# Kernel tuning notes

Measured on AMD Instinct MI355X. Metric: run time of the kernel, lower is better.

Reference implementation:

```python
import jax, jax.numpy as jnp
import numpy as np

D_MODEL = 1024
N_HEAD = 16
HEAD_DIM = D_MODEL // N_HEAD
BS, SEQ = 4, 2048
NEG_INF = -1e9


def setup_inputs() -> dict:
    key = jax.random.key(0)
    ks = jax.random.split(key, 10)
    X = jax.random.normal(ks[0], (BS, SEQ, D_MODEL), dtype=jnp.float32)
    kpm = jax.random.randint(ks[1], (BS, SEQ), 0, 2, dtype=jnp.int32)
    kpm = kpm.at[:, 0].set(0)  # guarantee at least one attendable key per batch
    scale = 1.0 / np.sqrt(D_MODEL)
    WQ = jax.random.normal(ks[2], (D_MODEL, D_MODEL), dtype=jnp.float32) * scale
    bQ = jnp.zeros((D_MODEL,), dtype=jnp.float32)
    WK = jax.random.normal(ks[3], (D_MODEL, D_MODEL), dtype=jnp.float32) * scale
    bK = jnp.zeros((D_MODEL,), dtype=jnp.float32)
    WV = jax.random.normal(ks[4], (D_MODEL, D_MODEL), dtype=jnp.float32) * scale
    bV = jnp.zeros((D_MODEL,), dtype=jnp.float32)
    WO = jax.random.normal(ks[5], (D_MODEL, D_MODEL), dtype=jnp.float32) * scale
    bO = jnp.zeros((D_MODEL,), dtype=jnp.float32)
    return {"X": X, "key_padding_mask": kpm, "WQ": WQ, "bQ": bQ,
            "WK": WK, "bK": bK, "WV": WV, "bV": bV, "WO": WO, "bO": bO}


def reference(X, key_padding_mask, WQ, bQ, WK, bK, WV, bV, WO, bO):
    bs, L, _ = X.shape
    # separate Q/K/V linear projections (torch Linear: x @ W.T + b)
    Q = X @ WQ.T + bQ
    K = X @ WK.T + bK
    V = X @ WV.T + bV
    # split heads: (bs, L, H, Dh) -> (bs, H, L, Dh)
    Q = Q.reshape(bs, L, N_HEAD, HEAD_DIM).transpose(0, 2, 1, 3)
    K = K.reshape(bs, L, N_HEAD, HEAD_DIM).transpose(0, 2, 1, 3)
    V = V.reshape(bs, L, N_HEAD, HEAD_DIM).transpose(0, 2, 1, 3)
    # scaled dot-product attention
    scores = jnp.einsum('bhqd,bhkd->bhqk', Q, K) / jnp.sqrt(
        jnp.asarray(HEAD_DIM, dtype=Q.dtype))
    # key padding mask: non-zero => ignore that key
    mask = (key_padding_mask != 0)[:, None, None, :]  # (bs,1,1,L)
    scores = jnp.where(mask, NEG_INF, scores)
    attn = jax.nn.softmax(scores, axis=-1)
    out = jnp.einsum('bhqk,bhkd->bhqd', attn, V)
    # merge heads
    out = out.transpose(0, 2, 1, 3).reshape(bs, L, D_MODEL)
    return out @ WO.T + bO
```

## Files before the change

### kernel.cpp

```cpp
#include <hip/hip_runtime.h>
#include <stdint.h>

#define BS_   4
#define SEQ_  2048
#define DM_   1024
#define NH_   16
#define DH_   64
#define MTOK_ (BS_*SEQ_)

typedef __attribute__((ext_vector_type(8))) short bf16x8;
typedef __attribute__((ext_vector_type(4))) float f32x4;

#define SA_ 0.18033688011112042f
#define SHIFT_ 16.0f

__device__ __forceinline__ unsigned short f2bf(float f) {
    union { float f; uint32_t u; } v; v.f = f;
    uint32_t r = v.u + 0x7fffu + ((v.u >> 16) & 1u);
    return (unsigned short)(r >> 16);
}

__device__ __forceinline__ float fexp2(float x) {
#if __has_builtin(__builtin_amdgcn_exp2f)
    return __builtin_amdgcn_exp2f(x);
#else
    return __expf(x * 0.69314718055994531f);
#endif
}

__device__ __forceinline__ uint32_t cvt_pk_bf16(float lo, float hi) {
    uint32_t r;
    asm("v_cvt_pk_bf16_f32 %0, %1, %2" : "=v"(r) : "v"(lo), "v"(hi));
    return r;
}

__device__ __forceinline__ void gload_lds16(const void* g, void* l) {
    __builtin_amdgcn_global_load_lds(
        (const __attribute__((address_space(1))) void*)g,
        (__attribute__((address_space(3))) void*)l, 16, 0, 0);
}

__global__ void cvt_kernel(const float* __restrict__ src,
                           unsigned short* __restrict__ dst, int n) {
    int i = (blockIdx.x * blockDim.x + threadIdx.x) * 4;
    const int stride = gridDim.x * blockDim.x * 4;
    for (; i < n; i += stride) {
        float4 v = *(const float4*)(src + i);
        ushort4 o;
        o.x = f2bf(v.x); o.y = f2bf(v.y); o.z = f2bf(v.z); o.w = f2bf(v.w);
        *(ushort4*)(dst + i) = o;
    }
}

__global__ void cvt4_kernel(const float* __restrict__ s0, const float* __restrict__ s1,
                            const float* __restrict__ s2, const float* __restrict__ s3,
                            unsigned short* __restrict__ dst) {
    const int i = (blockIdx.x * blockDim.x + threadIdx.x) * 4;
    const int mat = i >> 20;
    const int off = i & ((1 << 20) - 1);
    const float* s = (mat == 0) ? s0 : (mat == 1) ? s1 : (mat == 2) ? s2 : s3;
    float4 v = *(const float4*)(s + off);
    ushort4 o;
    o.x = f2bf(v.x); o.y = f2bf(v.y); o.z = f2bf(v.z); o.w = f2bf(v.w);
    *(ushort4*)(dst + i) = o;
}

template<int MODE>
__global__ __launch_bounds__(256) void gemm_bt(
    const unsigned short* __restrict__ A,
    const unsigned short* __restrict__ B,
    int Ndim, int Kdim,
    const float* __restrict__ bias0,
    const float* __restrict__ bias1,
    const float* __restrict__ bias2,
    unsigned short* __restrict__ Qo,
    unsigned short* __restrict__ Ko,
    unsigned short* __restrict__ Vt,
    float* __restrict__ Co)
{
    __shared__ unsigned short As[128 * 32];
    __shared__ unsigned short Bs[128 * 32];

    const int t    = threadIdx.x;
    const int lane = t & 63;
    const int w    = t >> 6;
    const int wr   = w >> 1, wc = w & 1;
    const int g    = lane >> 4, li = lane & 15;

    const int ntile = Ndim >> 7;
    const int per   = gridDim.x >> 3;
    const int sw    = (blockIdx.x & 7) * per + (blockIdx.x >> 3);
    const int tm = sw / ntile;
    const int tn = sw % ntile;

    const unsigned short* Ab = A + (size_t)tm * 128 * Kdim;
    const unsigned short* Bb = B + (size_t)tn * 128 * Kdim;

    f32x4 acc[4][4];
    const f32x4 zero = {0.f, 0.f, 0.f, 0.f};
    #pragma unroll
    for (int i = 0; i < 4; ++i)
        #pragma unroll
        for (int j = 0; j < 4; ++j)
            acc[i][j] = zero;

    const int s0 = t, s1 = t + 256;
    const int r0 = s0 >> 2, c0 = (s0 & 3) << 3;
    const int r1 = s1 >> 2, c1 = (s1 & 3) << 3;

    for (int k0 = 0; k0 < Kdim; k0 += 32) {
        gload_lds16(Ab + (size_t)r0 * Kdim + k0 + c0, (char*)As + s0 * 16);
        gload_lds16(Ab + (size_t)r1 * Kdim + k0 + c1, (char*)As + s1 * 16);
        gload_lds16(Bb + (size_t)r0 * Kdim + k0 + c0, (char*)Bs + s0 * 16);
        gload_lds16(Bb + (size_t)r1 * Kdim + k0 + c1, (char*)Bs + s1 * 16);
        __syncthreads();

        bf16x8 a[4], b[4];
        #pragma unroll
        for (int mi = 0; mi < 4; ++mi)
            a[mi] = *(const bf16x8*)&As[(wr * 64 + mi * 16 + li) * 32 + g * 8];
        #pragma unroll
        for (int ni = 0; ni < 4; ++ni)
            b[ni] = *(const bf16x8*)&Bs[(wc * 64 + ni * 16 + li) * 32 + g * 8];

        #pragma unroll
        for (int mi = 0; mi < 4; ++mi)
            #pragma unroll
            for (int ni = 0; ni < 4; ++ni)
                acc[mi][ni] = __builtin_amdgcn_mfma_f32_16x16x32_bf16(
                    a[mi], b[ni], acc[mi][ni], 0, 0, 0);
        __syncthreads();
    }

    if constexpr (MODE == 0) {
        #pragma unroll
        for (int mi = 0; mi < 4; ++mi) {
            const int gm0 = tm * 128 + wr * 64 + mi * 16 + g * 4;
            const int bb  = gm0 >> 11;
            const int l0  = gm0 & (SEQ_ - 1);
            #pragma unroll
            for (int ni = 0; ni < 4; ++ni) {
                const int gn  = tn * 128 + wc * 64 + ni * 16 + li;
                const int mat = gn >> 10;
                const int c   = gn & (DM_ - 1);
                const int hh  = c >> 6;
                const int dd  = c & (DH_ - 1);
                const float bias = (mat == 0 ? bias0 : (mat == 1 ? bias1 : bias2))[c];
                const f32x4 v = acc[mi][ni];
                if (mat == 2) {
                    const int lp = (l0 & ~31) | ((l0 & 12) << 1) | ((l0 & 16) >> 2);
                    ushort4 o;
                    o.x = f2bf(v[0] + bias);
                    o.y = f2bf(v[1] + bias);
                    o.z = f2bf(v[2] + bias);
                    o.w = f2bf(v[3] + bias);
                    *(ushort4*)&Vt[((size_t)(bb * NH_ + hh) * DH_ + dd) * SEQ_ + lp] = o;
                } else {
                    unsigned short* dst = (mat == 0) ? Qo : Ko;
                    #pragma unroll
                    for (int r = 0; r < 4; ++r)
                        dst[((size_t)(bb * NH_ + hh) * SEQ_ + l0 + r) * DH_ + dd] =
                            f2bf(v[r] + bias);
                }
            }
        }
    } else {
        #pragma unroll
        for (int mi = 0; mi < 4; ++mi) {
            const int gm0 = tm * 128 + wr * 64 + mi * 16 + g * 4;
            #pragma unroll
            for (int ni = 0; ni < 4; ++ni) {
                const int gn = tn * 128 + wc * 64 + ni * 16 + li;
                const float bias = bias0[gn];
                #pragma unroll
                for (int r = 0; r < 4; ++r)
                    Co[(size_t)(gm0 + r) * Ndim + gn] = acc[mi][ni][r] + bias;
            }
        }
    }
}

#define KPAD 72

__global__ __launch_bounds__(256) void attn_kernel(
    const unsigned short* __restrict__ Q,
    const unsigned short* __restrict__ K,
    const unsigned short* __restrict__ Vt,
    const int* __restrict__ kpm,
    unsigned short* __restrict__ Oo)
{
    __shared__ unsigned short Ks[64 * KPAD];
    __shared__ unsigned short Vs[64 * KPAD];
    __shared__ float maskLds[64];

    const int t    = threadIdx.x;
    const int lane = t & 63;
    const int w    = t >> 6;
    const int g    = lane >> 4, li = lane & 15;

    const int bh = ((blockIdx.x >> 7) << 3) + (blockIdx.x & 7);
    const int qt = (blockIdx.x >> 3) & 15;
    const int b  = bh >> 4;
    const int h  = bh & 15;
    const int q0 = qt * 128 + w * 32;

    bf16x8 qf[2][2];
    #pragma unroll
    for (int qi = 0; qi < 2; ++qi)
        #pragma unroll
        for (int kk = 0; kk < 2; ++kk)
            qf[qi][kk] = *(const bf16x8*)&Q[((size_t)bh * SEQ_ + q0 + qi * 16 + li) * DH_
                                            + kk * 32 + g * 8];

    f32x4 Oacc[2][4];
    const f32x4 zero = {0.f, 0.f, 0.f, 0.f};
    #pragma unroll
    for (int qi = 0; qi < 2; ++qi)
        #pragma unroll
        for (int di = 0; di < 4; ++di)
            Oacc[qi][di] = zero;

    float lrun[2] = {0.f, 0.f};

    const int sr = t >> 3;
    const int sc = (t & 7) * 8;

    bf16x8 kreg0, kreg1, vreg0, vreg1;
    float mreg = 0.f;

    auto load_tile = [&](int kv) {
        kreg0 = *(const bf16x8*)&K[((size_t)bh * SEQ_ + kv + sr) * DH_ + sc];
        kreg1 = *(const bf16x8*)&K[((size_t)bh * SEQ_ + kv + sr + 32) * DH_ + sc];
        vreg0 = *(const bf16x8*)&Vt[((size_t)bh * DH_ + sr) * SEQ_ + kv + sc];
        vreg1 = *(const bf16x8*)&Vt[((size_t)bh * DH_ + sr + 32) * SEQ_ + kv + sc];
        if (t < 64) mreg = (kpm[b * SEQ_ + kv + t] ? -1e9f : 0.0f) - SHIFT_;
    };
    auto store_tile = [&]() {
        *(bf16x8*)&Ks[sr * KPAD + sc] = kreg0;
        *(bf16x8*)&Ks[(sr + 32) * KPAD + sc] = kreg1;
        *(bf16x8*)&Vs[sr * KPAD + sc] = vreg0;
        *(bf16x8*)&Vs[(sr + 32) * KPAD + sc] = vreg1;
        if (t < 64) maskLds[t] = mreg;
    };

    load_tile(0);
    store_tile();

    for (int kv = 0; kv < SEQ_; kv += 64) {
        __syncthreads();
        const bool more = (kv + 64) < SEQ_;
        if (more) load_tile(kv + 64);

        float4 mk[4];
        #pragma unroll
        for (int ni = 0; ni < 4; ++ni)
            mk[ni] = *(const float4*)&maskLds[ni * 16 + g * 4];

        f32x4 sacc[2][4];
        #pragma unroll
        for (int qi = 0; qi < 2; ++qi)
            #pragma unroll
            for (int ni = 0; ni < 4; ++ni)
                sacc[qi][ni] = zero;
        __builtin_amdgcn_s_setprio(1);
        #pragma unroll
        for (int ni = 0; ni < 4; ++ni) {
            #pragma unroll
            for (int kk = 0; kk < 2; ++kk) {
                bf16x8 kb = *(const bf16x8*)&Ks[(ni * 16 + li) * KPAD + kk * 32 + g * 8];
                sacc[0][ni] = __builtin_amdgcn_mfma_f32_16x16x32_bf16(
                    kb, qf[0][kk], sacc[0][ni], 0, 0, 0);
                sacc[1][ni] = __builtin_amdgcn_mfma_f32_16x16x32_bf16(
                    kb, qf[1][kk], sacc[1][ni], 0, 0, 0);
            }
        }
        __builtin_amdgcn_s_setprio(0);

        #pragma unroll
        for (int qi = 0; qi < 2; ++qi) {
            float rs = 0.f;
            #pragma unroll
            for (int ni = 0; ni < 4; ++ni) {
                #pragma unroll
                for (int r = 0; r < 4; ++r) {
                    const float mval = (r == 0) ? mk[ni].x : (r == 1) ? mk[ni].y
                                      : (r == 2) ? mk[ni].z : mk[ni].w;
                    const float p = fexp2(fmaf(sacc[qi][ni][r], SA_, mval));
                    sacc[qi][ni][r] = p;
                    rs += p;
                }
            }
            lrun[qi] += rs;
        }

        bf16x8 pa[2][2];
        #pragma unroll
        for (int qi = 0; qi < 2; ++qi)
            #pragma unroll
            for (int kk = 0; kk < 2; ++kk) {
                union { bf16x8 v; uint32_t w4[4]; } u;
                u.w4[0] = cvt_pk_bf16(sacc[qi][2 * kk][0],     sacc[qi][2 * kk][1]);
                u.w4[1] = cvt_pk_bf16(sacc[qi][2 * kk][2],     sacc[qi][2 * kk][3]);
                u.w4[2] = cvt_pk_bf16(sacc[qi][2 * kk + 1][0], sacc[qi][2 * kk + 1][1]);
                u.w4[3] = cvt_pk_bf16(sacc[qi][2 * kk + 1][2], sacc[qi][2 * kk + 1][3]);
                pa[qi][kk] = u.v;
            }

        __builtin_amdgcn_s_setprio(1);
        #pragma unroll
        for (int di = 0; di < 4; ++di) {
            #pragma unroll
            for (int kk = 0; kk < 2; ++kk) {
                bf16x8 vb = *(const bf16x8*)&Vs[(di * 16 + li) * KPAD + kk * 32 + g * 8];
                Oacc[0][di] = __builtin_amdgcn_mfma_f32_16x16x32_bf16(
                    vb, pa[0][kk], Oacc[0][di], 0, 0, 0);
                Oacc[1][di] = __builtin_amdgcn_mfma_f32_16x16x32_bf16(
                    vb, pa[1][kk], Oacc[1][di], 0, 0, 0);
            }
        }
        __builtin_amdgcn_s_setprio(0);

        __syncthreads();
        if (more) store_tile();
    }

    #pragma unroll
    for (int qi = 0; qi < 2; ++qi) {
        float lt = lrun[qi];
        lt += __shfl_xor(lt, 16);
        lt += __shfl_xor(lt, 32);
        const float inv = 1.0f / lt;
        const int q = q0 + qi * 16 + li;
        #pragma unroll
        for (int di = 0; di < 4; ++di) {
            ushort4 o;
            o.x = f2bf(Oacc[qi][di][0] * inv);
            o.y = f2bf(Oacc[qi][di][1] * inv);
            o.z = f2bf(Oacc[qi][di][2] * inv);
            o.w = f2bf(Oacc[qi][di][3] * inv);
            *(ushort4*)&Oo[((size_t)b * SEQ_ + q) * DM_ + h * 64 + di * 16 + g * 4] = o;
        }
    }
}

extern "C" void kernel_launch(void* const* d_in, const int* in_sizes, int n_in,
                              void* d_out, int out_size, void* d_ws, size_t ws_size,
                              hipStream_t stream) {
    const float* X  = (const float*)d_in[0];
    const int*  kpm = (const int*)d_in[1];
    const float* WQ = (const float*)d_in[2];
    const float* bQ = (const float*)d_in[3];
    const float* WK = (const float*)d_in[4];
    const float* bK = (const float*)d_in[5];
    const float* WV = (const float*)d_in[6];
    const float* bV = (const float*)d_in[7];
    const float* WO = (const float*)d_in[8];
    const float* bO = (const float*)d_in[9];
    float* Out = (float*)d_out;

    char* ws = (char*)d_ws;
    unsigned short* Xb  = (unsigned short*)(ws);
    unsigned short* Wb  = (unsigned short*)(ws + (16u << 20));
    unsigned short* WOb = (unsigned short*)(ws + (22u << 20));
    unsigned short* Qb  = (unsigned short*)(ws + (24u << 20));
    unsigned short* Kb  = (unsigned short*)(ws + (40u << 20));
    unsigned short* Vtb = (unsigned short*)(ws + (56u << 20));
    unsigned short* AOb = Xb;

    cvt_kernel<<<2048, 256, 0, stream>>>(X, Xb, (int)(MTOK_ * DM_));
    cvt4_kernel<<<4096, 256, 0, stream>>>(WQ, WK, WV, WO, Wb);

    gemm_bt<0><<<(MTOK_ / 128) * (3 * DM_ / 128), 256, 0, stream>>>(
        Xb, Wb, 3 * DM_, DM_, bQ, bK, bV, Qb, Kb, Vtb, nullptr);

    attn_kernel<<<BS_ * NH_ * (SEQ_ / 128), 256, 0, stream>>>(Qb, Kb, Vtb, kpm, AOb);

    gemm_bt<1><<<(MTOK_ / 128) * (DM_ / 128), 256, 0, stream>>>(
        AOb, WOb, DM_, DM_, bO, nullptr, nullptr, nullptr, nullptr, nullptr, Out);
}
```

Baseline: 222.0 us.

## Software-pipeline attention loop: overlap next QK^T with current softmax and PV

Restructures the attention KV loop into a two-stage software pipeline. The QK^T MFMAs for tile i+1 are issued before the softmax and PV work for tile i, using ping-pong score registers and double-buffered V and mask shared memory. The aim is to let the exp/convert VALU work overlap with matrix-core work and hide LDS latency. The cost is higher register pressure from two score accumulators and more complex barrier placement.

```diff
diff --git a/kernel.cpp b/kernel.cpp
--- a/kernel.cpp
+++ b/kernel.cpp
@@ -181,6 +181,7 @@
 }
 
 #define KPAD 72
+#define NT_  (SEQ_ / 64)
 
 __global__ __launch_bounds__(256) void attn_kernel(
     const unsigned short* __restrict__ Q,
@@ -190,8 +191,8 @@
     unsigned short* __restrict__ Oo)
 {
     __shared__ unsigned short Ks[64 * KPAD];
-    __shared__ unsigned short Vs[64 * KPAD];
-    __shared__ float maskLds[64];
+    __shared__ unsigned short Vs[2][64 * KPAD];
+    __shared__ float maskLds[2][64];
 
     const int t    = threadIdx.x;
     const int lane = t & 63;
@@ -235,46 +236,40 @@
         vreg1 = *(const bf16x8*)&Vt[((size_t)bh * DH_ + sr + 32) * SEQ_ + kv + sc];
         if (t < 64) mreg = (kpm[b * SEQ_ + kv + t] ? -1e9f : 0.0f) - SHIFT_;
     };
-    auto store_tile = [&]() {
+    auto store_tile = [&](int buf) {
         *(bf16x8*)&Ks[sr * KPAD + sc] = kreg0;
         *(bf16x8*)&Ks[(sr + 32) * KPAD + sc] = kreg1;
-        *(bf16x8*)&Vs[sr * KPAD + sc] = vreg0;
-        *(bf16x8*)&Vs[(sr + 32) * KPAD + sc] = vreg1;
-        if (t < 64) maskLds[t] = mreg;
+        *(bf16x8*)&Vs[buf][sr * KPAD + sc] = vreg0;
+        *(bf16x8*)&Vs[buf][(sr + 32) * KPAD + sc] = vreg1;
+        if (t < 64) maskLds[buf][t] = mreg;
     };
 
-    load_tile(0);
-    store_tile();
-
-    for (int kv = 0; kv < SEQ_; kv += 64) {
-        __syncthreads();
-        const bool more = (kv + 64) < SEQ_;
-        if (more) load_tile(kv + 64);
-
-        float4 mk[4];
-        #pragma unroll
-        for (int ni = 0; ni < 4; ++ni)
-            mk[ni] = *(const float4*)&maskLds[ni * 16 + g * 4];
-
-        f32x4 sacc[2][4];
+    auto qk_phase = [&](f32x4 (&snew)[2][4]) {
         #pragma unroll
         for (int qi = 0; qi < 2; ++qi)
             #pragma unroll
             for (int ni = 0; ni < 4; ++ni)
-                sacc[qi][ni] = zero;
+                snew[qi][ni] = zero;
         __builtin_amdgcn_s_setprio(1);
         #pragma unroll
         for (int ni = 0; ni < 4; ++ni) {
             #pragma unroll
             for (int kk = 0; kk < 2; ++kk) {
                 bf16x8 kb = *(const bf16x8*)&Ks[(ni * 16 + li) * KPAD + kk * 32 + g * 8];
-                sacc[0][ni] = __builtin_amdgcn_mfma_f32_16x16x32_bf16(
-                    kb, qf[0][kk], sacc[0][ni], 0, 0, 0);
-                sacc[1][ni] = __builtin_amdgcn_mfma_f32_16x16x32_bf16(
-                    kb, qf[1][kk], sacc[1][ni], 0, 0, 0);
+                snew[0][ni] = __builtin_amdgcn_mfma_f32_16x16x32_bf16(
+                    kb, qf[0][kk], snew[0][ni], 0, 0, 0);
+                snew[1][ni] = __builtin_amdgcn_mfma_f32_16x16x32_bf16(
+                    kb, qf[1][kk], snew[1][ni], 0, 0, 0);
             }
         }
         __builtin_amdgcn_s_setprio(0);
+    };
+
+    auto smpv_phase = [&](f32x4 (&sold)[2][4], int pbuf) {
+        float4 mk[4];
+        #pragma unroll
+        for (int ni = 0; ni < 4; ++ni)
+            mk[ni] = *(const float4*)&maskLds[pbuf][ni * 16 + g * 4];
 
         #pragma unroll
         for (int qi = 0; qi < 2; ++qi) {
@@ -285,8 +280,8 @@
                 for (int r = 0; r < 4; ++r) {
                     const float mval = (r == 0) ? mk[ni].x : (r == 1) ? mk[ni].y
                                       : (r == 2) ? mk[ni].z : mk[ni].w;
-                    const float p = fexp2(fmaf(sacc[qi][ni][r], SA_, mval));
-                    sacc[qi][ni][r] = p;
+                    const float p = fexp2(fmaf(sold[qi][ni][r], SA_, mval));
+                    sold[qi][ni][r] = p;
                     rs += p;
                 }
             }
@@ -299,10 +294,10 @@
             #pragma unroll
             for (int kk = 0; kk < 2; ++kk) {
                 union { bf16x8 v; uint32_t w4[4]; } u;
-                u.w4[0] = cvt_pk_bf16(sacc[qi][2 * kk][0],     sacc[qi][2 * kk][1]);
-                u.w4[1] = cvt_pk_bf16(sacc[qi][2 * kk][2],     sacc[qi][2 * kk][3]);
-                u.w4[2] = cvt_pk_bf16(sacc[qi][2 * kk + 1][0], sacc[qi][2 * kk + 1][1]);
-                u.w4[3] = cvt_pk_bf16(sacc[qi][2 * kk + 1][2], sacc[qi][2 * kk + 1][3]);
+                u.w4[0] = cvt_pk_bf16(sold[qi][2 * kk][0],     sold[qi][2 * kk][1]);
+                u.w4[1] = cvt_pk_bf16(sold[qi][2 * kk][2],     sold[qi][2 * kk][3]);
+                u.w4[2] = cvt_pk_bf16(sold[qi][2 * kk + 1][0], sold[qi][2 * kk + 1][1]);
+                u.w4[3] = cvt_pk_bf16(sold[qi][2 * kk + 1][2], sold[qi][2 * kk + 1][3]);
                 pa[qi][kk] = u.v;
             }
 
@@ -311,7 +306,7 @@
         for (int di = 0; di < 4; ++di) {
             #pragma unroll
             for (int kk = 0; kk < 2; ++kk) {
-                bf16x8 vb = *(const bf16x8*)&Vs[(di * 16 + li) * KPAD + kk * 32 + g * 8];
+                bf16x8 vb = *(const bf16x8*)&Vs[pbuf][(di * 16 + li) * KPAD + kk * 32 + g * 8];
                 Oacc[0][di] = __builtin_amdgcn_mfma_f32_16x16x32_bf16(
                     vb, pa[0][kk], Oacc[0][di], 0, 0, 0);
                 Oacc[1][di] = __builtin_amdgcn_mfma_f32_16x16x32_bf16(
@@ -319,10 +314,38 @@
             }
         }
         __builtin_amdgcn_s_setprio(0);
-
-        __syncthreads();
-        if (more) store_tile();
+    };
+
+    f32x4 saccA[2][4], saccB[2][4];
+
+    load_tile(0);
+    store_tile(0);
+    __syncthreads();
+    qk_phase(saccA);
+    load_tile(64);
+    __syncthreads();
+    store_tile(1);
+
+    for (int tt = 1; tt + 1 < NT_; tt += 2) {
+        __syncthreads();
+        qk_phase(saccB);
+        load_tile((tt + 1) * 64);
+        smpv_phase(saccA, 0);
+        __syncthreads();
+        store_tile(0);
+
+        __syncthreads();
+        qk_phase(saccA);
+        if (tt + 2 < NT_) load_tile((tt + 2) * 64);
+        smpv_phase(saccB, 1);
+        __syncthreads();
+        if (tt + 2 < NT_) store_tile(1);
     }
+
+    __syncthreads();
+    qk_phase(saccB);
+    smpv_phase(saccA, 0);
+    smpv_phase(saccB, 1);
 
     #pragma unroll
     for (int qi = 0; qi < 2; ++qi) {
```

New measurement: 225.4 us. About the same (+1.5%).
